# Optimization experiments

Measured on AMD Instinct MI355X. Metric: run time of the kernel, lower is better.

## Reference

```python
import jax, jax.numpy as jnp
import numpy as np

B, L, D_MODEL, HEADS, EXP, DEPTH = 2, 2048, 1024, 16, 2, 12
D_EXP = D_MODEL * EXP
D_HEAD = D_EXP // HEADS


def _layernorm(x, g, b, eps=1e-5):
    mu = jnp.mean(x, axis=-1, keepdims=True)
    var = jnp.mean(jnp.square(x - mu), axis=-1, keepdims=True)
    return (x - mu) * jax.lax.rsqrt(var + eps) * g + b


def setup_inputs() -> dict:
    key = jax.random.key(0)
    ks = jax.random.split(key, 4)
    x = jax.random.normal(ks[0], (B, L, D_MODEL), dtype=jnp.float32)
    w_in = jax.random.normal(ks[1], (D_MODEL, 4 * D_EXP), dtype=jnp.float32) * 0.02
    w_out = jax.random.normal(ks[2], (D_EXP, D_MODEL), dtype=jnp.float32) * (0.02 / np.sqrt(2 * DEPTH))
    return {
        "x": x,
        "ln1_g": jnp.ones((D_MODEL,), jnp.float32),
        "ln1_b": jnp.zeros((D_MODEL,), jnp.float32),
        "ln2_g": jnp.ones((D_MODEL,), jnp.float32),
        "ln2_b": jnp.zeros((D_MODEL,), jnp.float32),
        "w_in": w_in,
        "w_out": w_out,
        "smear_factor": jnp.linspace(-6.0, 6.0, HEADS, dtype=jnp.float32),
        "log_scale": jnp.zeros((HEADS,), jnp.float32),
    }


def reference(x, ln1_g, ln1_b, ln2_g, ln2_b, w_in, w_out, smear_factor, log_scale):
    b, l, d = x.shape
    h = smear_factor.shape[0]
    d_exp = w_in.shape[1] // 4
    dh = d_exp // h

    qkvp = _layernorm(x, ln1_g, ln1_b) @ w_in  # [b, l, 4*d_exp]
    q, k, v, p = jnp.split(qkvp, 4, axis=-1)
    # 'b i (h d) -> b h i d'
    to_heads = lambda t: t.reshape(b, l, h, dh).transpose(0, 2, 1, 3)
    q, k, v = to_heads(q), to_heads(k), to_heads(v)

    # smeared keys: k_i <- (1-s)*k_i + s*k_{i-1}  (zero at i=0)
    smear = jax.nn.sigmoid(smear_factor)[None, :, None, None]
    k_prev = jnp.pad(k, ((0, 0), (0, 0), (1, 0), (0, 0)))[:, :, :-1, :]
    k = (1.0 - smear) * k + smear * k_prev

    # ALiBi-style additive mask: slope[h]*j on causal part, -1e10 above diag
    half = h // 2
    slopes = jnp.concatenate([2.0 ** jnp.linspace(0.0, -8.0, half), jnp.zeros((h - half,), jnp.float32)])
    j = jnp.arange(l)
    causal = jnp.where(j[None, :] > j[:, None], jnp.float32(-1e10), jnp.float32(0.0))  # [l, l]
    mask = slopes[:, None, None] * j[None, None, :].astype(jnp.float32) + causal[None, :, :]  # [h, l, l]

    # SDPA with q/s, k/s and default scale 1/sqrt(dh): logits = q k^T / (s^2 sqrt(dh))
    inv = 1.0 / (jnp.exp(2.0 * log_scale)[None, :, None, None] * jnp.sqrt(jnp.float32(dh)))
    logits = jnp.einsum('bhid,bhjd->bhij', q, k) * inv + mask[None]
    attn = jax.nn.softmax(logits, axis=-1)
    o = jnp.einsum('bhij,bhjd->bhid', attn, v)
    o = o.transpose(0, 2, 1, 3).reshape(b, l, h * dh)  # 'b h i d -> b i (h d)'

    out = (jax.nn.silu(p) * o) @ w_out
    return _layernorm(out, ln2_g, ln2_b)
```

## Files before the change

kernel.cpp:

```cpp
#include <hip/hip_runtime.h>

typedef unsigned short u16;
typedef __attribute__((ext_vector_type(8))) short bf16x8;
typedef __attribute__((ext_vector_type(8))) unsigned short u16x8;
typedef __attribute__((ext_vector_type(4))) float f32x4;

#define L_SEQ 2048
#define NTOK 4096
#define DMODEL 1024
#define DEXP 2048
#define NH 16
#define DH 128

__device__ __forceinline__ u16 f2bf(float f) {
    unsigned u = __float_as_uint(f);
    unsigned r = (u + 0x7FFFu + ((u >> 16) & 1u)) >> 16;
    return (u16)r;
}
__device__ __forceinline__ float bf2f(u16 h) {
    return __uint_as_float(((unsigned)h) << 16);
}

__device__ __forceinline__ void gl_lds16(const u16* g, u16* l) {
    __builtin_amdgcn_global_load_lds((const __attribute__((address_space(1))) void*)g,
                                     (__attribute__((address_space(3))) void*)l, 16, 0, 0);
}

__global__ void conv_transpose(const float* __restrict__ in, u16* __restrict__ out, int R, int C) {
    __shared__ unsigned tile[32][33];
    int c0 = blockIdx.x * 32, r0 = blockIdx.y * 32;
    int tx = threadIdx.x, ty = threadIdx.y;
    for (int j = 0; j < 32; j += 8)
        tile[ty + j][tx] = (unsigned)f2bf(in[(size_t)(r0 + ty + j) * C + c0 + tx]);
    __syncthreads();
    for (int j = 0; j < 32; j += 8)
        out[(size_t)(c0 + ty + j) * R + r0 + tx] = (u16)tile[tx][ty + j];
}

__global__ __launch_bounds__(256) void ln_fwd(const float* __restrict__ x, const float* __restrict__ g,
                                              const float* __restrict__ bta, void* __restrict__ outp,
                                              int out_bf16) {
    int row = blockIdx.x;
    int t = threadIdx.x;
    const float* xr = x + (size_t)row * DMODEL;
    float4 xv = *(const float4*)&xr[t * 4];
    float s = xv.x + xv.y + xv.z + xv.w;
    float s2 = xv.x * xv.x + xv.y * xv.y + xv.z * xv.z + xv.w * xv.w;
    for (int off = 32; off >= 1; off >>= 1) {
        s += __shfl_xor(s, off);
        s2 += __shfl_xor(s2, off);
    }
    __shared__ float red[10];
    int w = t >> 6;
    if ((t & 63) == 0) { red[w] = s; red[4 + w] = s2; }
    __syncthreads();
    if (t == 0) {
        red[8] = red[0] + red[1] + red[2] + red[3];
        red[9] = red[4] + red[5] + red[6] + red[7];
    }
    __syncthreads();
    float mu = red[8] * (1.0f / DMODEL);
    float var = red[9] * (1.0f / DMODEL) - mu * mu;
    float rstd = rsqrtf(var + 1e-5f);
    float vals[4] = {xv.x, xv.y, xv.z, xv.w};
    for (int e = 0; e < 4; e++) {
        int c = t * 4 + e;
        float y = (vals[e] - mu) * rstd * g[c] + bta[c];
        if (out_bf16) ((u16*)outp)[(size_t)row * DMODEL + c] = f2bf(y);
        else          ((float*)outp)[(size_t)row * DMODEL + c] = y;
    }
}

__global__ __launch_bounds__(512, 2) void gemm_8ph(const u16* __restrict__ A, const u16* __restrict__ BT,
                                                   u16* __restrict__ C, int M, int N, int K) {
    __shared__ u16 a_s[32768];
    __shared__ u16 b_s[32768];
    int tid = threadIdx.x;
    int w = tid >> 6, lane = tid & 63, quad = lane >> 4, ln = lane & 15;
    int lsw = ln & 7;
    int awrow = (w >> 2) * 64 + ln;
    int bwcol = (w & 3) * 32 + ln;

    unsigned lin = blockIdx.x + gridDim.x * blockIdx.y;
    unsigned per = gridDim.x >> 3;
    unsigned xcd = lin & 7, tt = lin >> 3;
    unsigned n_p = xcd * per + (tt % per);
    unsigned m_p = tt / per;
    int m0 = m_p * 256, n0 = n_p * 256;

    const u16 *Ah0[2], *Ah1[2], *Bh0[2], *Bh1[2];
    int ldoff[2];
#pragma unroll
    for (int j = 0; j < 2; j++) {
        int s = j * 512 + tid;
        int row = s >> 3, seg = s & 7;
        int sw = seg ^ (row & 7);
        Ah0[j] = A + (size_t)(m0 + row) * K + sw * 8;
        Ah1[j] = A + (size_t)(m0 + 128 + row) * K + sw * 8;
        Bh0[j] = BT + (size_t)(n0 + row) * K + sw * 8;
        Bh1[j] = BT + (size_t)(n0 + 128 + row) * K + sw * 8;
        ldoff[j] = (j * 512 + w * 64) * 8;
    }

    f32x4 zero4 = {0.f, 0.f, 0.f, 0.f};
    f32x4 acc[4][4][2];
#pragma unroll
    for (int q = 0; q < 4; q++)
#pragma unroll
        for (int fr = 0; fr < 4; fr++)
#pragma unroll
            for (int fc = 0; fc < 2; fc++) acc[q][fr][fc] = zero4;

    bf16x8 af_[4][2], bf_[2][2];

#define G1_STAGE(MS, PTRS, B, H, T)                                                   \
    do {                                                                              \
        _Pragma("unroll") for (int j = 0; j < 2; j++)                                 \
            gl_lds16(PTRS[j] + (size_t)(T) * 64, &MS[((B)*2 + (H)) * 8192 + ldoff[j]]); \
    } while (0)

#define G1_PHASE(BUF, QM, QN, DOA, DOB, STAGE_STMT, TAILGATE)                         \
    do {                                                                              \
        if (DOA) {                                                                    \
            _Pragma("unroll") for (int fr = 0; fr < 4; fr++)                          \
            _Pragma("unroll") for (int ks = 0; ks < 2; ks++)                          \
                af_[fr][ks] = *(const bf16x8*)&a_s[((BUF)*2 + (QM)) * 8192 +          \
                    (awrow + fr * 16) * 64 + (((ks * 4 + quad) ^ lsw) * 8)];          \
        }                                                                             \
        if (DOB) {                                                                    \
            _Pragma("unroll") for (int fc = 0; fc < 2; fc++)                          \
            _Pragma("unroll") for (int ks = 0; ks < 2; ks++)                          \
                bf_[fc][ks] = *(const bf16x8*)&b_s[((BUF)*2 + (QN)) * 8192 +          \
                    (bwcol + fc * 16) * 64 + (((ks * 4 + quad) ^ lsw) * 8)];          \
        }                                                                             \
        STAGE_STMT;                                                                   \
        __builtin_amdgcn_s_barrier();                                                 \
        asm volatile("s_waitcnt lgkmcnt(0)" ::: "memory");                            \
        __builtin_amdgcn_sched_barrier(0);                                            \
        __builtin_amdgcn_s_setprio(1);                                                \
        _Pragma("unroll") for (int fr = 0; fr < 4; fr++)                              \
        _Pragma("unroll") for (int fc = 0; fc < 2; fc++)                              \
        _Pragma("unroll") for (int ks = 0; ks < 2; ks++)                              \
            acc[(QM)*2 + (QN)][fr][fc] = __builtin_amdgcn_mfma_f32_16x16x32_bf16(     \
                af_[fr][ks], bf_[fc][ks], acc[(QM)*2 + (QN)][fr][fc], 0, 0, 0);       \
        __builtin_amdgcn_s_setprio(0);                                                \
        TAILGATE;                                                                     \
        __builtin_amdgcn_s_barrier();                                                 \
    } while (0)

    int NT = K >> 6;

    G1_STAGE(a_s, Ah0, 0, 0, 0);
    G1_STAGE(a_s, Ah1, 0, 1, 0);
    G1_STAGE(b_s, Bh0, 0, 0, 0);
    G1_STAGE(b_s, Bh1, 0, 1, 0);
    G1_STAGE(a_s, Ah0, 1, 0, 1);
    G1_STAGE(b_s, Bh1, 1, 1, 1);
    asm volatile("s_waitcnt vmcnt(4)" ::: "memory");
    __builtin_amdgcn_s_barrier();

    for (int t = 0; t < NT; t++) {
        int buf = t & 1, nb = buf ^ 1;
        G1_PHASE(buf, 0, 0, 1, 1, { if (t + 1 < NT) G1_STAGE(a_s, Ah1, nb, 1, t + 1); }, {});
        G1_PHASE(buf, 0, 1, 0, 1, { if (t + 1 < NT) G1_STAGE(b_s, Bh0, nb, 0, t + 1); }, {});
        G1_PHASE(buf, 1, 1, 1, 0, { if (t + 2 < NT) G1_STAGE(a_s, Ah0, buf, 0, t + 2); }, {});
        G1_PHASE(buf, 1, 0, 0, 1, { if (t + 2 < NT) G1_STAGE(b_s, Bh1, buf, 1, t + 2); },
                 {
                     if (t + 2 < NT) asm volatile("s_waitcnt vmcnt(4)" ::: "memory");
                     else            asm volatile("s_waitcnt vmcnt(0)" ::: "memory");
                 });
    }

#undef G1_STAGE
#undef G1_PHASE

#pragma unroll
    for (int QM = 0; QM < 2; QM++)
#pragma unroll
        for (int QN = 0; QN < 2; QN++)
#pragma unroll
            for (int fr = 0; fr < 4; fr++)
#pragma unroll
                for (int fc = 0; fc < 2; fc++)
#pragma unroll
                    for (int e = 0; e < 4; e++) {
                        int row = m0 + QM * 128 + (w >> 2) * 64 + fr * 16 + quad * 4 + e;
                        int col = n0 + QN * 128 + (w & 3) * 32 + fc * 16 + ln;
                        C[(size_t)row * N + col] = f2bf(acc[QM * 2 + QN][fr][fc][e]);
                    }
}

__global__ __launch_bounds__(256) void gemm_bt64(const u16* __restrict__ A, const u16* __restrict__ BT,
                                                 float* __restrict__ C, int M, int N, int K) {
    __shared__ u16 a_s[2][2048];
    __shared__ u16 b_s[2][4096];
    int tid = threadIdx.x;
    unsigned NX = gridDim.x;
    unsigned lin = blockIdx.x + NX * blockIdx.y;
    unsigned per = NX >> 3;
    unsigned xcd = lin & 7, t = lin >> 3;
    unsigned n_p = xcd * per + (t % per);
    unsigned m_p = t / per;
    int m0 = m_p * 64, n0 = n_p * 128;
    int w = tid >> 6, lane = tid & 63, quad = lane >> 4, ln = lane & 15;
    int wc = w * 32;
    f32x4 zero4 = {0.f, 0.f, 0.f, 0.f};
    f32x4 acc[4][2];
    for (int r = 0; r < 4; r++)
        for (int c = 0; c < 2; c++) acc[r][c] = zero4;

    int lrow = lane >> 2;
    int lseg = ((lane & 3) ^ ((lrow >> 1) & 3)) * 8;
    int qsw = (quad ^ ((ln >> 1) & 3)) * 8;
    const u16* Ag  = A + (size_t)(m0 + 16 * w + lrow) * K + lseg;
    const u16* Bg0 = BT + (size_t)(n0 + 32 * w + lrow) * K + lseg;
    const u16* Bg1 = Bg0 + (size_t)16 * K;
    int la = w * 512;
    int lb0 = (2 * w) * 512, lb1 = (2 * w + 1) * 512;

    gl_lds16(Ag, &a_s[0][la]);
    gl_lds16(Bg0, &b_s[0][lb0]);
    gl_lds16(Bg1, &b_s[0][lb1]);
    __syncthreads();

    int cur = 0;
    for (int k0 = 0; k0 < K; k0 += 32) {
        if (k0 + 32 < K) {
            int nb = cur ^ 1;
            gl_lds16(Ag + k0 + 32, &a_s[nb][la]);
            gl_lds16(Bg0 + k0 + 32, &b_s[nb][lb0]);
            gl_lds16(Bg1 + k0 + 32, &b_s[nb][lb1]);
        }
        bf16x8 af[4], bfr[2];
        for (int r = 0; r < 4; r++) af[r]  = *(const bf16x8*)&a_s[cur][(r * 16 + ln) * 32 + qsw];
        for (int c = 0; c < 2; c++) bfr[c] = *(const bf16x8*)&b_s[cur][(wc + c * 16 + ln) * 32 + qsw];
        __builtin_amdgcn_s_setprio(1);
        for (int r = 0; r < 4; r++)
            for (int c = 0; c < 2; c++)
                acc[r][c] = __builtin_amdgcn_mfma_f32_16x16x32_bf16(af[r], bfr[c], acc[r][c], 0, 0, 0);
        __builtin_amdgcn_s_setprio(0);
        __syncthreads();
        cur ^= 1;
    }
    for (int r = 0; r < 4; r++)
        for (int c = 0; c < 2; c++)
            for (int e = 0; e < 4; e++) {
                int row = m0 + r * 16 + quad * 4 + e;
                int col = n0 + wc + c * 16 + ln;
                C[(size_t)row * N + col] = acc[r][c][e];
            }
}

__global__ __launch_bounds__(256) void smear_kernel(const u16* __restrict__ qkvp,
                                                    const float* __restrict__ smear_f,
                                                    u16* __restrict__ k_sm) {
    int gid = blockIdx.x * 256 + threadIdx.x;
    int base = gid * 8;
    int bl = base >> 11;
    int c = base & 2047;
    int h = c >> 7;
    int d = c & 127;
    int l = bl & (L_SEQ - 1);
    int bb = bl >> 11;
    float s = 1.0f / (1.0f + __expf(-smear_f[h]));
    u16x8 cur = *(const u16x8*)&qkvp[(size_t)bl * 8192 + 2048 + c];
    u16x8 prv = {0, 0, 0, 0, 0, 0, 0, 0};
    if (l > 0) prv = *(const u16x8*)&qkvp[(size_t)(bl - 1) * 8192 + 2048 + c];
    u16x8 outv;
    for (int u = 0; u < 8; u++) {
        float kc = bf2f(cur[u]);
        float kp = bf2f(prv[u]);
        outv[u] = f2bf((1.0f - s) * kc + s * kp);
    }
    *(u16x8*)&k_sm[(((size_t)(bb * 16 + h)) * L_SEQ + l) * DH + d] = outv;
}

__global__ void vT_kernel(const u16* __restrict__ qkvp, u16* __restrict__ v_t) {
    __shared__ unsigned tile[32][33];
    int l0 = blockIdx.x * 32, d0 = blockIdx.y * 32;
    int bh = blockIdx.z;
    int bb = bh >> 4, h = bh & 15;
    int tx = threadIdx.x, ty = threadIdx.y;
    size_t tokb = (size_t)bb * L_SEQ;
    for (int j = 0; j < 32; j += 8)
        tile[ty + j][tx] = (unsigned)qkvp[(tokb + l0 + ty + j) * 8192 + 4096 + h * DH + d0 + tx];
    __syncthreads();
    for (int j = 0; j < 32; j += 8)
        v_t[((size_t)bh * DH + d0 + ty + j) * L_SEQ + l0 + tx] = (u16)tile[tx][ty + j];
}

__global__ __launch_bounds__(256) void attn_kernel(const u16* __restrict__ qkvp,
                                                   const u16* __restrict__ k_sm,
                                                   const u16* __restrict__ v_t,
                                                   u16* __restrict__ ag2,
                                                   const float* __restrict__ log_scale) {
    __shared__ u16 k_s[16384];
    __shared__ u16 vt_s[16384];
    __shared__ u16 p_s[4608];
    int tid = threadIdx.x;
    unsigned lin = blockIdx.x + 16u * blockIdx.y;
    unsigned xcd = lin & 7, tt = lin >> 3;
    int bh = (int)(xcd * 4 + (tt & 3));
    int pair = (int)(tt >> 2);
    int bb = bh >> 4, h = bh & 15;
    int w = tid >> 6, lane = tid & 63, quad = lane >> 4, ln = lane & 15;
    size_t tokb = (size_t)bb * L_SEQ;

    const float LOG2E = 1.44269504f;
    float inv = 1.0f / (__expf(2.0f * log_scale[h]) * sqrtf((float)DH));
    float scl = inv * LOG2E;
    float slope2 = ((h < 8) ? exp2f(-8.0f * (float)h / 7.0f) : 0.0f) * LOG2E;

    int lrow = lane >> 2, lcol = lane & 3;
    int lsw8 = (lcol ^ ((lrow >> 1) & 3)) * 8;
    int qsw = (quad ^ ((ln >> 1) & 3)) * 8;
    f32x4 zero4 = {0.f, 0.f, 0.f, 0.f};
    u16* pw = &p_s[w * 1152];
    const short ONE_BF = (short)0x3F80;
    bf16x8 ones = {ONE_BF, ONE_BF, ONE_BF, ONE_BF, ONE_BF, ONE_BF, ONE_BF, ONE_BF};

    for (int sidx = 0; sidx < 2; sidx++) {
        int ib = sidx == 0 ? (31 - pair) : pair;
        int i0 = ib * 64;
        int si = i0 + w * 16;
        int iq = si + ln;

        bf16x8 qf[4];
        for (int kt = 0; kt < 4; kt++)
            qf[kt] = *(const bf16x8*)&qkvp[(tokb + si + ln) * 8192 + h * DH + kt * 32 + quad * 8];

        float mshift = -1e30f;
        float astep = slope2 * 64.0f;
        f32x4 o_acc[8], l_acc;
        for (int dt = 0; dt < 8; dt++) o_acc[dt] = zero4;
        l_acc = zero4;

        float adt0[4][4];
        for (int ct = 0; ct < 4; ct++)
            for (int r = 0; r < 4; r++)
                adt0[ct][r] = slope2 * (float)(ct * 16 + quad * 4 + r);

        const u16* kg[4];
        for (int g = 0; g < 4; g++)
            kg[g] = k_sm + ((size_t)bh * L_SEQ + g * 16 + lrow) * DH + w * 32 + lsw8;
        const u16* vg[4];
        int vloff[4];
        for (int q = 0; q < 4; q++) {
            int c = w * 4 + q;
            int jt = c >> 3, dg = c & 7;
            vg[q] = v_t + ((size_t)bh * DH + dg * 16 + lrow) * L_SEQ + jt * 32 + lsw8;
            vloff[q] = jt * 4096 + dg * 512;
        }

        for (int g = 0; g < 4; g++) { gl_lds16(kg[g], &k_s[w * 2048 + g * 512]); kg[g] += 64 * DH; }
        for (int q = 0; q < 4; q++) { gl_lds16(vg[q], &vt_s[vloff[q]]); vg[q] += 64; }
        __syncthreads();

        int cur = 0;
        for (int j0 = 0; j0 <= i0; j0 += 64) {
            if (j0 + 64 <= i0) {
                int nb = (cur ^ 1) * 8192;
                for (int g = 0; g < 4; g++) { gl_lds16(kg[g], &k_s[nb + w * 2048 + g * 512]); kg[g] += 64 * DH; }
                for (int q = 0; q < 4; q++) { gl_lds16(vg[q], &vt_s[nb + vloff[q]]); vg[q] += 64; }
            }
            const u16* kb = &k_s[cur * 8192];
            const u16* vb = &vt_s[cur * 8192];

            f32x4 sc[4];
            for (int ct = 0; ct < 4; ct++) sc[ct] = zero4;
            __builtin_amdgcn_s_setprio(1);
            for (int kt = 0; kt < 4; kt++)
                for (int ct = 0; ct < 4; ct++) {
                    bf16x8 bfr = *(const bf16x8*)&kb[kt * 2048 + (ct * 16 + ln) * 32 + qsw];
                    sc[ct] = __builtin_amdgcn_mfma_f32_16x16x32_bf16(bfr, qf[kt], sc[ct], 0, 0, 0);
                }
            __builtin_amdgcn_s_setprio(0);

            bool full = (j0 + 63 <= si);
            float s2[4][4];
            for (int ct = 0; ct < 4; ct++)
                for (int r = 0; r < 4; r++) {
                    float v = fmaf(sc[ct][r], scl, adt0[ct][r]);
                    if (!full) {
                        int j = j0 + ct * 16 + quad * 4 + r;
                        if (j > iq) v = -3.0e38f;
                    }
                    s2[ct][r] = v;
                }
            float x0 = fmaxf(fmaxf(s2[0][0], s2[0][1]), s2[0][2]);
            float x1 = fmaxf(fmaxf(s2[0][3], s2[1][0]), s2[1][1]);
            float x2 = fmaxf(fmaxf(s2[1][2], s2[1][3]), s2[2][0]);
            float x3 = fmaxf(fmaxf(s2[2][1], s2[2][2]), s2[2][3]);
            float x4 = fmaxf(fmaxf(s2[3][0], s2[3][1]), s2[3][2]);
            float y0 = fmaxf(fmaxf(x0, x1), x2);
            float y1 = fmaxf(fmaxf(x3, x4), s2[3][3]);
            float mr = fmaxf(y0, y1);
            mr = fmaxf(mr, __shfl_xor(mr, 16));
            mr = fmaxf(mr, __shfl_xor(mr, 32));
            float msh_old = mshift - astep;
            float mnew = fmaxf(msh_old, mr);
            float alpha = exp2f(msh_old - mnew);
            mshift = mnew;

            for (int ct = 0; ct < 4; ct++) {
                float p0 = exp2f(s2[ct][0] - mnew);
                float p1 = exp2f(s2[ct][1] - mnew);
                float p2 = exp2f(s2[ct][2] - mnew);
                float p3 = exp2f(s2[ct][3] - mnew);
                unsigned d0 = __builtin_amdgcn_perm(__float_as_uint(p1), __float_as_uint(p0), 0x07060302u);
                unsigned d1 = __builtin_amdgcn_perm(__float_as_uint(p3), __float_as_uint(p2), 0x07060302u);
                uint2 dd; dd.x = d0; dd.y = d1;
                *(uint2*)&pw[ln * 72 + ct * 16 + quad * 4] = dd;
            }

            if (__any(alpha != 1.0f)) {
                float av[4];
                for (int e = 0; e < 4; e++) av[e] = __shfl(alpha, quad * 20 + e);
                for (int dt = 0; dt < 8; dt++) {
                    f32x4 o = o_acc[dt];
                    for (int e = 0; e < 4; e++) o[e] *= av[e];
                    o_acc[dt] = o;
                }
                for (int e = 0; e < 4; e++) l_acc[e] *= av[e];
            }
            asm volatile("s_waitcnt lgkmcnt(0)" ::: "memory");
            __builtin_amdgcn_s_setprio(1);
            for (int ks = 0; ks < 2; ks++) {
                bf16x8 pa = *(const bf16x8*)&pw[ln * 72 + ks * 32 + quad * 8];
                l_acc = __builtin_amdgcn_mfma_f32_16x16x32_bf16(pa, ones, l_acc, 0, 0, 0);
                for (int dt = 0; dt < 8; dt++) {
                    bf16x8 vf = *(const bf16x8*)&vb[ks * 4096 + (dt * 16 + ln) * 32 + qsw];
                    o_acc[dt] = __builtin_amdgcn_mfma_f32_16x16x32_bf16(pa, vf, o_acc[dt], 0, 0, 0);
                }
            }
            __builtin_amdgcn_s_setprio(0);
            __syncthreads();
            cur ^= 1;
        }

        float rinv[4];
        for (int r = 0; r < 4; r++) rinv[r] = __builtin_amdgcn_rcpf(l_acc[r]);
        for (int dt = 0; dt < 8; dt++)
            for (int r = 0; r < 4; r++) {
                int i = si + quad * 4 + r;
                int dcol = dt * 16 + ln;
                float o = o_acc[dt][r] * rinv[r];
                float pv = bf2f(qkvp[(tokb + i) * 8192 + 6144 + h * DH + dcol]);
                float gate = pv * __builtin_amdgcn_rcpf(1.0f + exp2f(-pv * LOG2E));
                ag2[(tokb + i) * 2048 + h * DH + dcol] = f2bf(gate * o);
            }
    }
}

extern "C" void kernel_launch(void* const* d_in, const int* in_sizes, int n_in,
                              void* d_out, int out_size, void* d_ws, size_t ws_size,
                              hipStream_t stream) {
    const float* x       = (const float*)d_in[0];
    const float* ln1_g   = (const float*)d_in[1];
    const float* ln1_b   = (const float*)d_in[2];
    const float* ln2_g   = (const float*)d_in[3];
    const float* ln2_b   = (const float*)d_in[4];
    const float* w_in    = (const float*)d_in[5];
    const float* w_out   = (const float*)d_in[6];
    const float* smear_f = (const float*)d_in[7];
    const float* logsc   = (const float*)d_in[8];
    float* out = (float*)d_out;
    char* ws = (char*)d_ws;

    u16* w_inT   = (u16*)(ws + 0);
    u16* w_outT  = (u16*)(ws + (size_t)16777216);
    u16* lnA     = (u16*)(ws + (size_t)20971520);
    u16* qkvp    = (u16*)(ws + (size_t)29360128);
    u16* k_sm    = (u16*)(ws + (size_t)96468992);
    u16* ag2     = (u16*)(ws + (size_t)113246208);
    float* out_pre = (float*)(ws + (size_t)96468992);
    u16* v_t     = (u16*)(ws + 0);

    dim3 b32x8(32, 8);
    conv_transpose<<<dim3(8192 / 32, 1024 / 32), b32x8, 0, stream>>>(w_in, w_inT, 1024, 8192);
    conv_transpose<<<dim3(1024 / 32, 2048 / 32), b32x8, 0, stream>>>(w_out, w_outT, 2048, 1024);
    ln_fwd<<<NTOK, 256, 0, stream>>>(x, ln1_g, ln1_b, (void*)lnA, 1);
    gemm_8ph<<<dim3(8192 / 256, 4096 / 256), 512, 0, stream>>>(lnA, w_inT, qkvp, NTOK, 8192, 1024);
    smear_kernel<<<4096, 256, 0, stream>>>(qkvp, smear_f, k_sm);
    vT_kernel<<<dim3(L_SEQ / 32, DH / 32, 32), b32x8, 0, stream>>>(qkvp, v_t);
    attn_kernel<<<dim3(16, 32), 256, 0, stream>>>(qkvp, k_sm, v_t, ag2, logsc);
    gemm_bt64<<<dim3(1024 / 128, 4096 / 64), 256, 0, stream>>>(ag2, w_outT, out_pre, NTOK, 1024, 2048);
    ln_fwd<<<NTOK, 256, 0, stream>>>(out_pre, ln2_g, ln2_b, (void*)out, 0);
}
```

Measured before the change: 335.7 us.

## Double K-step in output GEMM and merge smear with V transpose kernel

The output-projection GEMM now loads 64-wide K slices per stage instead of 32, with a new XOR swizzle over 8 segments. Each stage issues twice the MFMAs, so there are half as many barriers and loop iterations, at the cost of twice the LDS per block. Separately, the key-smear and V-transpose kernels are merged into one launch, with an extra grid slice handling the smear. This removes one kernel launch and its tail.

```diff
diff --git a/kernel.cpp b/kernel.cpp
--- a/kernel.cpp
+++ b/kernel.cpp
@@ -192,8 +192,8 @@
 
 __global__ __launch_bounds__(256) void gemm_bt64(const u16* __restrict__ A, const u16* __restrict__ BT,
                                                  float* __restrict__ C, int M, int N, int K) {
-    __shared__ u16 a_s[2][2048];
-    __shared__ u16 b_s[2][4096];
+    __shared__ u16 a_s[2][4096];
+    __shared__ u16 b_s[2][8192];
     int tid = threadIdx.x;
     unsigned NX = gridDim.x;
     unsigned lin = blockIdx.x + NX * blockIdx.y;
@@ -203,41 +203,61 @@
     unsigned m_p = t / per;
     int m0 = m_p * 64, n0 = n_p * 128;
     int w = tid >> 6, lane = tid & 63, quad = lane >> 4, ln = lane & 15;
-    int wc = w * 32;
+    int wc = w * 32, lsw = ln & 7;
     f32x4 zero4 = {0.f, 0.f, 0.f, 0.f};
     f32x4 acc[4][2];
     for (int r = 0; r < 4; r++)
         for (int c = 0; c < 2; c++) acc[r][c] = zero4;
 
-    int lrow = lane >> 2;
-    int lseg = ((lane & 3) ^ ((lrow >> 1) & 3)) * 8;
-    int qsw = (quad ^ ((ln >> 1) & 3)) * 8;
-    const u16* Ag  = A + (size_t)(m0 + 16 * w + lrow) * K + lseg;
-    const u16* Bg0 = BT + (size_t)(n0 + 32 * w + lrow) * K + lseg;
-    const u16* Bg1 = Bg0 + (size_t)16 * K;
-    int la = w * 512;
-    int lb0 = (2 * w) * 512, lb1 = (2 * w + 1) * 512;
-
-    gl_lds16(Ag, &a_s[0][la]);
-    gl_lds16(Bg0, &b_s[0][lb0]);
-    gl_lds16(Bg1, &b_s[0][lb1]);
+    const u16* Ag[2];
+    int aoff[2];
+#pragma unroll
+    for (int j = 0; j < 2; j++) {
+        int s = j * 256 + tid;
+        int row = s >> 3, seg = s & 7;
+        Ag[j] = A + (size_t)(m0 + row) * K + (seg ^ (row & 7)) * 8;
+        aoff[j] = s * 8;
+    }
+    const u16* Bg[4];
+    int boff[4];
+#pragma unroll
+    for (int j = 0; j < 4; j++) {
+        int s = j * 256 + tid;
+        int row = s >> 3, seg = s & 7;
+        Bg[j] = BT + (size_t)(n0 + row) * K + (seg ^ (row & 7)) * 8;
+        boff[j] = s * 8;
+    }
+
+    for (int j = 0; j < 2; j++) gl_lds16(Ag[j], &a_s[0][aoff[j]]);
+    for (int j = 0; j < 4; j++) gl_lds16(Bg[j], &b_s[0][boff[j]]);
     __syncthreads();
 
     int cur = 0;
-    for (int k0 = 0; k0 < K; k0 += 32) {
-        if (k0 + 32 < K) {
+    for (int k0 = 0; k0 < K; k0 += 64) {
+        if (k0 + 64 < K) {
             int nb = cur ^ 1;
-            gl_lds16(Ag + k0 + 32, &a_s[nb][la]);
-            gl_lds16(Bg0 + k0 + 32, &b_s[nb][lb0]);
-            gl_lds16(Bg1 + k0 + 32, &b_s[nb][lb1]);
+            for (int j = 0; j < 2; j++) gl_lds16(Ag[j] + k0 + 64, &a_s[nb][aoff[j]]);
+            for (int j = 0; j < 4; j++) gl_lds16(Bg[j] + k0 + 64, &b_s[nb][boff[j]]);
         }
-        bf16x8 af[4], bfr[2];
-        for (int r = 0; r < 4; r++) af[r]  = *(const bf16x8*)&a_s[cur][(r * 16 + ln) * 32 + qsw];
-        for (int c = 0; c < 2; c++) bfr[c] = *(const bf16x8*)&b_s[cur][(wc + c * 16 + ln) * 32 + qsw];
+        bf16x8 af[4][2], bfr[2][2];
+#pragma unroll
+        for (int r = 0; r < 4; r++)
+#pragma unroll
+            for (int ks = 0; ks < 2; ks++)
+                af[r][ks] = *(const bf16x8*)&a_s[cur][(r * 16 + ln) * 64 + (((ks * 4 + quad) ^ lsw) * 8)];
+#pragma unroll
+        for (int c = 0; c < 2; c++)
+#pragma unroll
+            for (int ks = 0; ks < 2; ks++)
+                bfr[c][ks] = *(const bf16x8*)&b_s[cur][(wc + c * 16 + ln) * 64 + (((ks * 4 + quad) ^ lsw) * 8)];
         __builtin_amdgcn_s_setprio(1);
+#pragma unroll
         for (int r = 0; r < 4; r++)
+#pragma unroll
             for (int c = 0; c < 2; c++)
-                acc[r][c] = __builtin_amdgcn_mfma_f32_16x16x32_bf16(af[r], bfr[c], acc[r][c], 0, 0, 0);
+#pragma unroll
+                for (int ks = 0; ks < 2; ks++)
+                    acc[r][c] = __builtin_amdgcn_mfma_f32_16x16x32_bf16(af[r][ks], bfr[c][ks], acc[r][c], 0, 0, 0);
         __builtin_amdgcn_s_setprio(0);
         __syncthreads();
         cur ^= 1;
@@ -251,42 +271,41 @@
             }
 }
 
-__global__ __launch_bounds__(256) void smear_kernel(const u16* __restrict__ qkvp,
-                                                    const float* __restrict__ smear_f,
-                                                    u16* __restrict__ k_sm) {
-    int gid = blockIdx.x * 256 + threadIdx.x;
-    int base = gid * 8;
-    int bl = base >> 11;
-    int c = base & 2047;
-    int h = c >> 7;
-    int d = c & 127;
-    int l = bl & (L_SEQ - 1);
-    int bb = bl >> 11;
-    float s = 1.0f / (1.0f + __expf(-smear_f[h]));
-    u16x8 cur = *(const u16x8*)&qkvp[(size_t)bl * 8192 + 2048 + c];
-    u16x8 prv = {0, 0, 0, 0, 0, 0, 0, 0};
-    if (l > 0) prv = *(const u16x8*)&qkvp[(size_t)(bl - 1) * 8192 + 2048 + c];
-    u16x8 outv;
-    for (int u = 0; u < 8; u++) {
-        float kc = bf2f(cur[u]);
-        float kp = bf2f(prv[u]);
-        outv[u] = f2bf((1.0f - s) * kc + s * kp);
-    }
-    *(u16x8*)&k_sm[(((size_t)(bb * 16 + h)) * L_SEQ + l) * DH + d] = outv;
-}
-
-__global__ void vT_kernel(const u16* __restrict__ qkvp, u16* __restrict__ v_t) {
+__global__ void vT_smear(const u16* __restrict__ qkvp, const float* __restrict__ smear_f,
+                         u16* __restrict__ v_t, u16* __restrict__ k_sm) {
     __shared__ unsigned tile[32][33];
-    int l0 = blockIdx.x * 32, d0 = blockIdx.y * 32;
     int bh = blockIdx.z;
     int bb = bh >> 4, h = bh & 15;
     int tx = threadIdx.x, ty = threadIdx.y;
     size_t tokb = (size_t)bb * L_SEQ;
-    for (int j = 0; j < 32; j += 8)
-        tile[ty + j][tx] = (unsigned)qkvp[(tokb + l0 + ty + j) * 8192 + 4096 + h * DH + d0 + tx];
-    __syncthreads();
-    for (int j = 0; j < 32; j += 8)
-        v_t[((size_t)bh * DH + d0 + ty + j) * L_SEQ + l0 + tx] = (u16)tile[tx][ty + j];
+    if (blockIdx.y < 4) {
+        int l0 = blockIdx.x * 32, d0 = blockIdx.y * 32;
+        for (int j = 0; j < 32; j += 8)
+            tile[ty + j][tx] = (unsigned)qkvp[(tokb + l0 + ty + j) * 8192 + 4096 + h * DH + d0 + tx];
+        __syncthreads();
+        for (int j = 0; j < 32; j += 8)
+            v_t[((size_t)bh * DH + d0 + ty + j) * L_SEQ + l0 + tx] = (u16)tile[tx][ty + j];
+    } else {
+        int l0 = blockIdx.x * 32;
+        int tid = ty * 32 + tx;
+        float s = 1.0f / (1.0f + __expf(-smear_f[h]));
+        for (int p = 0; p < 2; p++) {
+            int v = tid + p * 256;
+            int lr = v >> 4;
+            int d = (v & 15) * 8;
+            int l = l0 + lr;
+            u16x8 cur = *(const u16x8*)&qkvp[(tokb + l) * 8192 + 2048 + h * DH + d];
+            u16x8 prv = {0, 0, 0, 0, 0, 0, 0, 0};
+            if (l > 0) prv = *(const u16x8*)&qkvp[(tokb + l - 1) * 8192 + 2048 + h * DH + d];
+            u16x8 outv;
+            for (int u = 0; u < 8; u++) {
+                float kc = bf2f(cur[u]);
+                float kp = bf2f(prv[u]);
+                outv[u] = f2bf((1.0f - s) * kc + s * kp);
+            }
+            *(u16x8*)&k_sm[(((size_t)bh) * L_SEQ + l) * DH + d] = outv;
+        }
+    }
 }
 
 __global__ __launch_bounds__(256) void attn_kernel(const u16* __restrict__ qkvp,
@@ -481,8 +500,7 @@
     conv_transpose<<<dim3(1024 / 32, 2048 / 32), b32x8, 0, stream>>>(w_out, w_outT, 2048, 1024);
     ln_fwd<<<NTOK, 256, 0, stream>>>(x, ln1_g, ln1_b, (void*)lnA, 1);
     gemm_8ph<<<dim3(8192 / 256, 4096 / 256), 512, 0, stream>>>(lnA, w_inT, qkvp, NTOK, 8192, 1024);
-    smear_kernel<<<4096, 256, 0, stream>>>(qkvp, smear_f, k_sm);
-    vT_kernel<<<dim3(L_SEQ / 32, DH / 32, 32), b32x8, 0, stream>>>(qkvp, v_t);
+    vT_smear<<<dim3(L_SEQ / 32, 5, 32), b32x8, 0, stream>>>(qkvp, smear_f, v_t, k_sm);
     attn_kernel<<<dim3(16, 32), 256, 0, stream>>>(qkvp, k_sm, v_t, ag2, logsc);
     gemm_bt64<<<dim3(1024 / 128, 4096 / 64), 256, 0, stream>>>(ag2, w_outT, out_pre, NTOK, 1024, 2048);
     ln_fwd<<<NTOK, 256, 0, stream>>>(out_pre, ln2_g, ln2_b, (void*)out, 0);
```

Result: faster. 327.5 us (median of 2 runs) (-2.5%).
